# Kernel optimization log

Hardware: AMD Instinct MI355X
Metric: run time of the kernel (lower is better)

The kernel has to match this reference:

```python
import jax, jax.numpy as jnp
import numpy as np

B, L, H, KV, D, HID = 2, 2048, 16, 4, 128, 2048
EPS = 1e-6
ROPE_BASE = 10000.0


def _rotate_half(x):
    x1, x2 = jnp.split(x, 2, axis=-1)
    return jnp.concatenate((-x2, x1), axis=-1)


def _rms_norm(x, w):
    xf = x.astype(jnp.float32)
    var = jnp.mean(xf * xf, axis=-1, keepdims=True)
    return w * (xf * jax.lax.rsqrt(var + EPS)).astype(x.dtype)


def setup_inputs() -> dict:
    key = jax.random.key(0)
    ks = jax.random.split(key, 6)
    hidden_states = jax.random.normal(ks[0], (B, L, HID), dtype=jnp.float32)
    # rotary embeddings (standard rope table)
    inv_freq = 1.0 / (ROPE_BASE ** (jnp.arange(0, D, 2, dtype=jnp.float32) / D))
    pos = jnp.arange(L, dtype=jnp.float32)
    freqs = pos[:, None] * inv_freq[None, :]          # [L, D/2]
    emb = jnp.concatenate((freqs, freqs), axis=-1)    # [L, D]
    cos = jnp.broadcast_to(jnp.cos(emb)[None], (B, L, D))
    sin = jnp.broadcast_to(jnp.sin(emb)[None], (B, L, D))
    s = 0.02
    Wq = jax.random.normal(ks[1], (HID, H * D), dtype=jnp.float32) * s
    Wk = jax.random.normal(ks[2], (HID, KV * D), dtype=jnp.float32) * s
    Wv = jax.random.normal(ks[3], (HID, KV * D), dtype=jnp.float32) * s
    Wo = jax.random.normal(ks[4], (H * D, HID), dtype=jnp.float32) * s
    q_norm_w = jnp.ones((D,), dtype=jnp.float32)
    k_norm_w = jnp.ones((D,), dtype=jnp.float32)
    return {"hidden_states": hidden_states, "cos": cos, "sin": sin,
            "Wq": Wq, "Wk": Wk, "Wv": Wv, "Wo": Wo,
            "q_norm_w": q_norm_w, "k_norm_w": k_norm_w}


def reference(hidden_states, cos, sin, Wq, Wk, Wv, Wo, q_norm_w, k_norm_w):
    scale = D ** -0.5
    n_rep = H // KV
    q = (hidden_states @ Wq).reshape(B, L, H, D)
    k = (hidden_states @ Wk).reshape(B, L, KV, D)
    v = (hidden_states @ Wv).reshape(B, L, KV, D)
    q = _rms_norm(q, q_norm_w).transpose(0, 2, 1, 3)   # [B,H,L,D]
    k = _rms_norm(k, k_norm_w).transpose(0, 2, 1, 3)   # [B,KV,L,D]
    v = v.transpose(0, 2, 1, 3)                         # [B,KV,L,D]
    c = cos[:, None]                                    # [B,1,L,D]
    s = sin[:, None]
    q = q * c + _rotate_half(q) * s
    k = k * c + _rotate_half(k) * s
    # GQA without materializing repeated K/V: group query heads per kv head.
    qg = q.reshape(B, KV, n_rep, L, D)
    scores = jnp.einsum('bgrld,bgmd->bgrlm', qg, k) * scale
    attn = jax.nn.softmax(scores, axis=-1)
    out = jnp.einsum('bgrlm,bgmd->bgrld', attn, v)      # [B,KV,n_rep,L,D]
    out = out.reshape(B, H, L, D).transpose(0, 2, 1, 3).reshape(B, L, H * D)
    return out @ Wo
```

## Files before the change

kernel.cpp:

```cpp
#include <hip/hip_runtime.h>

typedef unsigned short u16;
typedef unsigned int u32;
typedef short bf16x8 __attribute__((ext_vector_type(8)));
typedef float f32x4 __attribute__((ext_vector_type(4)));

#define B_ 2
#define L_ 2048
#define H_ 16
#define KV_ 4
#define D_ 128
#define HID_ 2048

#define QSCALE (0.08838834764831845f * 1.4426950408889634f)

__device__ __forceinline__ u16 f2bf(float f) {
  union { float f; u32 u; } v; v.f = f;
  u32 u = v.u;
  return (u16)((u + 0x7FFFu + ((u >> 16) & 1u)) >> 16);
}
__device__ __forceinline__ float bf2f(u16 h) {
  union { u32 u; float f; } v; v.u = ((u32)h) << 16;
  return v.f;
}
__device__ __forceinline__ u32 pkbf(float a, float b) {
  union { float f; u32 u; } x, y; x.f = a; y.f = b;
  return ((x.u + 0x8000u) >> 16) | ((y.u + 0x8000u) & 0xffff0000u);
}
__device__ __forceinline__ void gl_lds16(const void* g, void* l) {
  __builtin_amdgcn_global_load_lds((__attribute__((address_space(1))) void*)(g),
                                   (__attribute__((address_space(3))) void*)(l),
                                   16, 0, 0);
}

template <int N> __device__ __forceinline__ void vmwait() {
  asm volatile("s_waitcnt vmcnt(%0)" ::"n"(N) : "memory");
}
#define BARRIER()                                                         \
  do {                                                                    \
    asm volatile("" ::: "memory");                                        \
    __builtin_amdgcn_s_barrier();                                         \
    asm volatile("" ::: "memory");                                        \
    __builtin_amdgcn_sched_barrier(0);                                    \
  } while (0)

__global__ void k_prep(const float* __restrict__ hidden, u16* __restrict__ Xb,
                       const float* __restrict__ Wq, const float* __restrict__ Wk,
                       const float* __restrict__ Wv, const float* __restrict__ Wo,
                       u16* __restrict__ Wtqkv, u16* __restrict__ Wto) {
  __shared__ float t[32][33];
  int id = blockIdx.x;
  if (id < 8192) {
    int i = id * 256 + threadIdx.x;
    float4 v = ((const float4*)hidden)[i];
    u32 a = (u32)f2bf(v.x) | ((u32)f2bf(v.y) << 16);
    u32 b = (u32)f2bf(v.z) | ((u32)f2bf(v.w) << 16);
    ((uint2*)Xb)[i] = make_uint2(a, b);
    return;
  }
  id -= 8192;
  const float* src; u16* dst; int C; int ct, rt;
  if (id < 4096)      { src = Wq; dst = Wtqkv;               C = 2048; ct = id & 63; rt = id >> 6; }
  else if (id < 5120) { id -= 4096; src = Wk; dst = Wtqkv + 2048 * 2048; C = 512; ct = id & 15; rt = id >> 4; }
  else if (id < 6144) { id -= 5120; src = Wv; dst = Wtqkv + 2560 * 2048; C = 512; ct = id & 15; rt = id >> 4; }
  else                { id -= 6144; src = Wo; dst = Wto;     C = 2048; ct = id & 63; rt = id >> 6; }
  const int R = 2048;
  int c0 = ct * 32, r0 = rt * 32;
  int tx = threadIdx.x & 31, ty = threadIdx.x >> 5;
  for (int i = ty; i < 32; i += 8)
    t[i][tx] = src[(size_t)(r0 + i) * C + c0 + tx];
  __syncthreads();
  int sc = threadIdx.x >> 3;
  int tg = threadIdx.x & 7;
  u32 lo = (u32)f2bf(t[tg * 4 + 0][sc]) | ((u32)f2bf(t[tg * 4 + 1][sc]) << 16);
  u32 hi = (u32)f2bf(t[tg * 4 + 2][sc]) | ((u32)f2bf(t[tg * 4 + 3][sc]) << 16);
  *(uint2*)(dst + (size_t)(c0 + sc) * R + r0 + tg * 4) = make_uint2(lo, hi);
}

__global__ __launch_bounds__(512, 2) void k_gemm_qkv(
    const u16* __restrict__ A, const u16* __restrict__ Bt,
    const float* __restrict__ cosp, const float* __restrict__ sinp,
    const float* __restrict__ qw, const float* __restrict__ kw,
    u16* __restrict__ Qb, u16* __restrict__ Kb, u16* __restrict__ Vtb) {
  extern __shared__ char smem[];
  const int tid = threadIdx.x;
  const int wave = tid >> 6, lane = tid & 63;
  const int wm = wave >> 2, wn = wave & 3;
  const int quad = lane >> 4, fm = lane & 15;
  const int f7 = fm & 7;

  const int bid = blockIdx.x;
  const int swz = (bid & 7) * 24 + (bid >> 3);
  const int by = swz / 12, bx = swz % 12;
  const int m0 = by * 256, n0 = bx * 256;

  const u16* Ag = A + (size_t)m0 * 2048;
  const u16* Bg = Bt + (size_t)n0 * 2048;
  const int schunk = (lane & 7) ^ ((lane >> 3) & 7);

  f32x4 acc[8][4];
#pragma unroll
  for (int i = 0; i < 8; ++i)
#pragma unroll
    for (int j = 0; j < 4; ++j)
#pragma unroll
      for (int r = 0; r < 4; ++r) acc[i][j][r] = 0.0f;

  bf16x8 af[4][2], bf[4][2];
  const int ArowB = (wm * 128 + fm) * 128;
  const int BrowB = (wn * 64 + fm) * 128;
  const int kc[2] = {(quad ^ f7) * 16, ((quad ^ 4) ^ f7) * 16};

#define STAGE_A(qa_, kk_, bb_)                                               \
  _Pragma("unroll") for (int q = 0; q < 2; ++q) {                            \
    int ldsoff = (bb_)*32768 + q * 16384 + (qa_)*8192 + wave * 1024 + lane * 16; \
    int grow = q * 128 + (qa_)*64 + wave * 8 + (lane >> 3);                  \
    gl_lds16(Ag + (size_t)grow * 2048 + (kk_)*64 + schunk * 8, smem + ldsoff); \
  }
#define STAGE_B(qb_, kk_, bb_)                                               \
  _Pragma("unroll") for (int q = 0; q < 2; ++q) {                            \
    int gg = q * 2 + (wave >> 2);                                            \
    int ldsoff = 65536 + (bb_)*32768 + gg * 8192 + (qb_)*4096 +              \
                 (wave & 3) * 1024 + lane * 16;                              \
    int grow = gg * 64 + (qb_)*32 + (wave & 3) * 8 + (lane >> 3);            \
    gl_lds16(Bg + (size_t)grow * 2048 + (kk_)*64 + schunk * 8, smem + ldsoff); \
  }
#define LDA4(bb_, roff_)                                                     \
  _Pragma("unroll") for (int i = 0; i < 4; ++i)                              \
    _Pragma("unroll") for (int ks = 0; ks < 2; ++ks)                         \
      af[i][ks] = *(const bf16x8*)(smem + (bb_)*32768 + ArowB + (roff_) +    \
                                   i * 2048 + kc[ks]);
#define LDB2(bb_, j0_)                                                       \
  _Pragma("unroll") for (int j = 0; j < 2; ++j)                              \
    _Pragma("unroll") for (int ks = 0; ks < 2; ++ks)                         \
      bf[(j0_) + j][ks] = *(const bf16x8*)(smem + 65536 + (bb_)*32768 +      \
                                           BrowB + ((j0_) + j) * 2048 + kc[ks]);
#define MFMA_Q(I0_, J0_)                                                     \
  __builtin_amdgcn_s_setprio(1);                                             \
  _Pragma("unroll") for (int i = 0; i < 4; ++i)                              \
    _Pragma("unroll") for (int j = 0; j < 2; ++j)                            \
      _Pragma("unroll") for (int ks = 0; ks < 2; ++ks)                       \
        acc[(I0_) + i][(J0_) + j] = __builtin_amdgcn_mfma_f32_16x16x32_bf16( \
            af[i][ks], bf[(J0_) + j][ks], acc[(I0_) + i][(J0_) + j], 0, 0, 0); \
  __builtin_amdgcn_s_setprio(0);
#define TILE(kt_, bb_, ST_, W0_, W1_, W2_)                                   \
  {                                                                          \
    vmwait<W0_>(); BARRIER();                                                \
    LDA4(bb_, 0); LDB2(bb_, 0);                                              \
    if (ST_) { STAGE_A(0, (kt_) + 1, (bb_) ^ 1); }                           \
    MFMA_Q(0, 0);                                                            \
    vmwait<W1_>(); BARRIER();                                                \
    LDB2(bb_, 2);                                                            \
    if (ST_) { STAGE_B(0, (kt_) + 1, (bb_) ^ 1); }                           \
    MFMA_Q(0, 2);                                                            \
    vmwait<W2_>(); BARRIER();                                                \
    LDA4(bb_, 8192);                                                         \
    if (ST_) { STAGE_B(1, (kt_) + 1, (bb_) ^ 1); }                           \
    MFMA_Q(4, 0);                                                            \
    if (ST_) { STAGE_A(1, (kt_) + 1, (bb_) ^ 1); }                           \
    MFMA_Q(4, 2);                                                            \
  }

  STAGE_A(0, 0, 0);
  STAGE_B(0, 0, 0);
  STAGE_B(1, 0, 0);
  STAGE_A(1, 0, 0);

#pragma unroll 1
  for (int t2 = 0; t2 < 30; t2 += 2) {
    TILE(t2, 0, 1, 4, 4, 4);
    TILE(t2 + 1, 1, 1, 4, 4, 4);
  }
  TILE(30, 0, 1, 4, 4, 4);
  TILE(31, 1, 0, 4, 2, 0);

#undef TILE
#undef MFMA_Q
#undef LDB2
#undef LDA4
#undef STAGE_B
#undef STAGE_A

  u16* Cs = (u16*)smem;
  const int head2 = bx * 2;
  const int bL = by >> 3;
  const int l0 = m0 & 2047;
  __syncthreads();
#pragma unroll 1
  for (int qq = 0; qq < 4; ++qq) {
    const int qm = qq >> 1, qn = qq & 1;
    __syncthreads();
    if (wm == qm && (wn >> 1) == qn) {
#pragma unroll
      for (int i = 0; i < 8; ++i)
#pragma unroll
        for (int j = 0; j < 4; ++j)
#pragma unroll
          for (int r = 0; r < 4; ++r)
            Cs[(i * 16 + quad * 4 + r) * 136 + (wn & 1) * 64 + j * 16 + fm] =
                f2bf(acc[i][j][r]);
    }
    __syncthreads();
    const int hq = head2 + qn;
    const int tok0 = m0 + qm * 128;
    const int l0q = l0 + qm * 128;
    if (hq < 20) {
      const int isq = hq < 16;
      const float* wv = isq ? qw : kw;
      const int half = lane >> 5, sl = lane & 31;
      u16* outp = isq ? (Qb + (size_t)(bL * H_ + hq) * L_ * D_)
                      : (Kb + (size_t)(bL * KV_ + hq - 16) * L_ * D_);
      const float4 wvv = *(const float4*)(wv + sl * 4);
      for (int it = 0; it < 8; ++it) {
        int r = wave * 16 + it * 2 + half;
        const u16* crow = Cs + r * 136 + sl * 4;
        u32 c01 = *(const u32*)crow;
        u32 c23 = *(const u32*)(crow + 2);
        float x0 = bf2f((u16)(c01 & 0xffff)), x1 = bf2f((u16)(c01 >> 16));
        float x2 = bf2f((u16)(c23 & 0xffff)), x3 = bf2f((u16)(c23 >> 16));
        float ssq = (x0 * x0 + x1 * x1) + (x2 * x2 + x3 * x3);
        ssq += __shfl_xor(ssq, 1);
        ssq += __shfl_xor(ssq, 2);
        ssq += __shfl_xor(ssq, 4);
        ssq += __shfl_xor(ssq, 8);
        ssq += __shfl_xor(ssq, 16);
        float rr = rsqrtf(ssq * (1.0f / 128.0f) + 1e-6f);
        float nn0 = x0 * rr * wvv.x, nn1 = x1 * rr * wvv.y;
        float nn2 = x2 * rr * wvv.z, nn3 = x3 * rr * wvv.w;
        float p0 = __shfl_xor(nn0, 16), p1 = __shfl_xor(nn1, 16);
        float p2 = __shfl_xor(nn2, 16), p3 = __shfl_xor(nn3, 16);
        float sgn = (sl < 16) ? -1.0f : 1.0f;
        int tok = tok0 + r;
        const float4 cv = *(const float4*)(cosp + (size_t)tok * 128 + sl * 4);
        const float4 sv = *(const float4*)(sinp + (size_t)tok * 128 + sl * 4);
        float o0 = nn0 * cv.x + sgn * p0 * sv.x;
        float o1 = nn1 * cv.y + sgn * p1 * sv.y;
        float o2 = nn2 * cv.z + sgn * p2 * sv.z;
        float o3 = nn3 * cv.w + sgn * p3 * sv.w;
        if (isq) { o0 *= QSCALE; o1 *= QSCALE; o2 *= QSCALE; o3 *= QSCALE; }
        u32 lo = (u32)f2bf(o0) | ((u32)f2bf(o1) << 16);
        u32 hi = (u32)f2bf(o2) | ((u32)f2bf(o3) << 16);
        *(uint2*)(outp + (size_t)(l0q + r) * D_ + sl * 4) = make_uint2(lo, hi);
      }
    } else {
      int g = hq - 20;
      int d = tid >> 2, a2 = (tid >> 1) & 1, lh = tid & 1;
      u16* dst = Vtb + ((size_t)(bL * KV_ + g) * D_ + d) * L_ + l0q + lh * 64;
      for (int bc = 0; bc < 8; ++bc) {
        int b2 = bc & 1, c = bc >> 1;
        int ls = lh * 64 + a2 * 32 + 16 * b2 + 4 * c;
        u32 lo = (u32)Cs[ls * 136 + d] | ((u32)Cs[(ls + 1) * 136 + d] << 16);
        u32 hi = (u32)Cs[(ls + 2) * 136 + d] | ((u32)Cs[(ls + 3) * 136 + d] << 16);
        *(uint2*)(dst + a2 * 32 + 8 * c + 4 * b2) = make_uint2(lo, hi);
      }
    }
  }
}

template <int OUT_BF16>
__global__ __launch_bounds__(256, 3) void k_gemm_bt(
    const u16* __restrict__ A, const u16* __restrict__ Bt, void* __restrict__ Cv,
    int M, int N, int K) {
  __shared__ u16 smem2[16384];
  u16* As = smem2;
  u16* Bs = smem2 + 8192;
  const int tid = threadIdx.x;
  const int wave = tid >> 6, lane = tid & 63;
  const int wr = wave >> 1, wc = wave & 1;
  const int quad = lane >> 4, fm = lane & 15;
  const int m0 = blockIdx.y * 128, n0 = blockIdx.x * 128;
  f32x4 acc[4][4];
  for (int i = 0; i < 4; ++i)
    for (int j = 0; j < 4; ++j)
      for (int r = 0; r < 4; ++r) acc[i][j][r] = 0.0f;

  const int lrow = lane >> 3;
  const int lcol = (lane & 7) * 8;
  const int fk = quad * 8;

  for (int kt = 0; kt < K; kt += 64) {
    for (int p = 0; p < 4; ++p) {
      int roff = wave * 32 + p * 8 + lrow;
      gl_lds16(A + (size_t)(m0 + roff) * K + kt + lcol,
               As + wave * 2048 + p * 512 + lane * 8);
      gl_lds16(Bt + (size_t)(n0 + roff) * K + kt + lcol,
               Bs + wave * 2048 + p * 512 + lane * 8);
    }
    __syncthreads();
    for (int s = 0; s < 2; ++s) {
      bf16x8 af[4], bfr[4];
      for (int i = 0; i < 4; ++i)
        af[i] = *(const bf16x8*)(As + (wr * 64 + i * 16 + fm) * 64 + s * 32 + fk);
      for (int j = 0; j < 4; ++j)
        bfr[j] = *(const bf16x8*)(Bs + (wc * 64 + j * 16 + fm) * 64 + s * 32 + fk);
      for (int i = 0; i < 4; ++i)
        for (int j = 0; j < 4; ++j)
          acc[i][j] = __builtin_amdgcn_mfma_f32_16x16x32_bf16(af[i], bfr[j],
                                                              acc[i][j], 0, 0, 0);
    }
    __syncthreads();
  }

  if (OUT_BF16) {
    u16* Cs = smem2;
    for (int hh = 0; hh < 2; ++hh) {
      if (hh) __syncthreads();
      if (wr == hh)
        for (int i = 0; i < 4; ++i)
          for (int j = 0; j < 4; ++j)
            for (int r = 0; r < 4; ++r)
              Cs[(i * 16 + quad * 4 + r) * 136 + wc * 64 + j * 16 + fm] =
                  f2bf(acc[i][j][r]);
      __syncthreads();
      for (int it = 0; it < 4; ++it) {
        int row = it * 16 + (tid >> 4);
        int col = (tid & 15) * 8;
        uint4 v = *(const uint4*)(Cs + row * 136 + col);
        *(uint4*)((u16*)Cv + (size_t)(m0 + hh * 64 + row) * N + n0 + col) = v;
      }
    }
  } else {
    float* Cf = (float*)Cv;
#pragma unroll
    for (int i = 0; i < 4; ++i)
#pragma unroll
      for (int j = 0; j < 4; ++j)
#pragma unroll
        for (int r = 0; r < 4; ++r)
          Cf[(size_t)(m0 + wr * 64 + i * 16 + quad * 4 + r) * N + n0 + wc * 64 +
             j * 16 + fm] = acc[i][j][r];
  }
}

__global__ __launch_bounds__(256, 2) void k_attn(const u16* __restrict__ Qb,
                                                 const u16* __restrict__ Kb,
                                                 const u16* __restrict__ Vtb,
                                                 u16* __restrict__ AO) {
  __shared__ u16 smem3[32768];
  const int tid = threadIdx.x, wave = tid >> 6, lane = tid & 63;
  const int quad = lane >> 4, fm = lane & 15;
  const int f7 = fm & 7;
  const int bid = blockIdx.x;
  const int xcd = bid & 7, w = bid >> 3;
  const int b = xcd >> 2, g = xcd & 3;
  const int h = g * 4 + (w & 3);
  const int qt = w >> 2;
  const int bh = b * 16 + h;
  const u16* Kg = Kb + ((size_t)(b * KV_ + g)) * L_ * D_;
  const u16* Vg = Vtb + ((size_t)(b * KV_ + g)) * D_ * L_;

  const u16* Qg = Qb + ((size_t)bh * L_ + qt * 128 + wave * 32 + fm) * D_;
  bf16x8 qf1[4], qf2[4];
  for (int ks = 0; ks < 4; ++ks) {
    qf1[ks] = *(const bf16x8*)(Qg + ks * 32 + quad * 8);
    qf2[ks] = *(const bf16x8*)(Qg + 16 * D_ + ks * 32 + quad * 8);
  }

  f32x4 o1[8], o2[8];
  for (int f = 0; f < 8; ++f)
    for (int r = 0; r < 4; ++r) { o1[f][r] = 0.0f; o2[f][r] = 0.0f; }
  float lr1 = 0.0f, lr2 = 0.0f;
  const f32x4 fz = {0.0f, 0.0f, 0.0f, 0.0f};

  const int eK = wave * 2048 + (lane << 3);
  const int cK = lane & 15;
  const int cV = lane & 7;

#define STAGE(kt_, buf_)                                                      \
  {                                                                           \
    u16* Kd = smem3 + (buf_)*16384;                                           \
    u16* Vd = smem3 + (buf_)*16384 + 8192;                                    \
    for (int p = 0; p < 4; ++p) {                                             \
      int e = eK + p * 512;                                                   \
      int rowK = e >> 7;                                                      \
      int gK = (cK & 8) | ((cK & 7) ^ (rowK & 7));                            \
      gl_lds16(Kg + (size_t)((kt_)*64 + rowK) * 128 + gK * 8, Kd + e);        \
      int rowV = e >> 6;                                                      \
      int gV = cV ^ (rowV & 7);                                               \
      gl_lds16(Vg + (size_t)rowV * L_ + (kt_)*64 + gV * 8, Vd + e);           \
    }                                                                         \
  }

  STAGE(0, 0);
  for (int kt = 0; kt < 32; ++kt) {
    __syncthreads();
    if (kt + 1 < 32) STAGE(kt + 1, (kt + 1) & 1);
    const u16* Ks = smem3 + (kt & 1) * 16384;
    const u16* Vs = Ks + 8192;

    f32x4 s1[4], s2[4];
    __builtin_amdgcn_s_setprio(1);
    {
      int cp = (quad & 8) | (quad ^ f7);
      for (int n = 0; n < 4; ++n) {
        bf16x8 kf = *(const bf16x8*)(Ks + (n * 16 + fm) * 128 + cp * 8);
        s1[n] = __builtin_amdgcn_mfma_f32_16x16x32_bf16(kf, qf1[0], fz, 0, 0, 0);
        s2[n] = __builtin_amdgcn_mfma_f32_16x16x32_bf16(kf, qf2[0], fz, 0, 0, 0);
      }
    }
    for (int ks = 1; ks < 4; ++ks) {
      int c = 4 * ks + quad;
      int cp = (c & 8) | ((c & 7) ^ f7);
      for (int n = 0; n < 4; ++n) {
        bf16x8 kf = *(const bf16x8*)(Ks + (n * 16 + fm) * 128 + cp * 8);
        s1[n] = __builtin_amdgcn_mfma_f32_16x16x32_bf16(kf, qf1[ks], s1[n], 0, 0, 0);
        s2[n] = __builtin_amdgcn_mfma_f32_16x16x32_bf16(kf, qf2[ks], s2[n], 0, 0, 0);
      }
    }
    __builtin_amdgcn_s_setprio(0);

    u32 pk1[4][2], pk2[4][2];
    float rs1 = 0.0f, rs2 = 0.0f;
    for (int n = 0; n < 4; ++n) {
      float a0 = __builtin_amdgcn_exp2f(s1[n][0]);
      float a1 = __builtin_amdgcn_exp2f(s1[n][1]);
      float a2 = __builtin_amdgcn_exp2f(s1[n][2]);
      float a3 = __builtin_amdgcn_exp2f(s1[n][3]);
      rs1 += (a0 + a1) + (a2 + a3);
      pk1[n][0] = pkbf(a0, a1);
      pk1[n][1] = pkbf(a2, a3);
      float b0 = __builtin_amdgcn_exp2f(s2[n][0]);
      float b1 = __builtin_amdgcn_exp2f(s2[n][1]);
      float b2 = __builtin_amdgcn_exp2f(s2[n][2]);
      float b3 = __builtin_amdgcn_exp2f(s2[n][3]);
      rs2 += (b0 + b1) + (b2 + b3);
      pk2[n][0] = pkbf(b0, b1);
      pk2[n][1] = pkbf(b2, b3);
    }
    lr1 += rs1;
    lr2 += rs2;

    __builtin_amdgcn_s_setprio(1);
    for (int ks2 = 0; ks2 < 2; ++ks2) {
      union { u32 u[4]; bf16x8 v; } pa1, pa2;
      pa1.u[0] = pk1[2 * ks2][0];
      pa1.u[1] = pk1[2 * ks2][1];
      pa1.u[2] = pk1[2 * ks2 + 1][0];
      pa1.u[3] = pk1[2 * ks2 + 1][1];
      pa2.u[0] = pk2[2 * ks2][0];
      pa2.u[1] = pk2[2 * ks2][1];
      pa2.u[2] = pk2[2 * ks2 + 1][0];
      pa2.u[3] = pk2[2 * ks2 + 1][1];
      int chunk = (4 * ks2 + quad) ^ f7;
      for (int f = 0; f < 8; ++f) {
        bf16x8 vv = *(const bf16x8*)(Vs + (f * 16 + fm) * 64 + chunk * 8);
        o1[f] = __builtin_amdgcn_mfma_f32_16x16x32_bf16(pa1.v, vv, o1[f], 0, 0, 0);
        o2[f] = __builtin_amdgcn_mfma_f32_16x16x32_bf16(pa2.v, vv, o2[f], 0, 0, 0);
      }
    }
    __builtin_amdgcn_s_setprio(0);
  }
#undef STAGE

  const size_t tok0 = (size_t)b * L_ + qt * 128;
  for (int grp = 0; grp < 2; ++grp) {
    f32x4* o = grp ? o2 : o1;
    float lr = grp ? lr2 : lr1;
    lr += __shfl_xor(lr, 16);
    lr += __shfl_xor(lr, 32);
    float li = 1.0f / lr;
    float l0 = __shfl(li, (lane & 48) | (quad * 4 + 0));
    float l1 = __shfl(li, (lane & 48) | (quad * 4 + 1));
    float l2 = __shfl(li, (lane & 48) | (quad * 4 + 2));
    float l3 = __shfl(li, (lane & 48) | (quad * 4 + 3));
    __syncthreads();
    for (int f = 0; f < 8; ++f) {
      int e = (wave * 16 + quad * 4) * 136 + f * 16 + fm;
      smem3[e] = f2bf(o[f][0] * l0);
      smem3[e + 136] = f2bf(o[f][1] * l1);
      smem3[e + 272] = f2bf(o[f][2] * l2);
      smem3[e + 408] = f2bf(o[f][3] * l3);
    }
    __syncthreads();
    for (int it = 0; it < 8; ++it) {
      int crow = (tid >> 6) * 16 + it * 2 + (lane >> 5);
      int q = (crow >> 4) * 32 + grp * 16 + (crow & 15);
      int cc = (lane & 31) * 4;
      uint2 v = *(const uint2*)(smem3 + crow * 136 + cc);
      *(uint2*)(AO + (tok0 + q) * (H_ * D_) + h * D_ + cc) = v;
    }
  }
}

extern "C" void kernel_launch(void* const* d_in, const int* in_sizes, int n_in,
                              void* d_out, int out_size, void* d_ws,
                              size_t ws_size, hipStream_t stream) {
  const float* hidden = (const float*)d_in[0];
  const float* cosp = (const float*)d_in[1];
  const float* sinp = (const float*)d_in[2];
  const float* Wq = (const float*)d_in[3];
  const float* Wk = (const float*)d_in[4];
  const float* Wv = (const float*)d_in[5];
  const float* Wo = (const float*)d_in[6];
  const float* qw = (const float*)d_in[7];
  const float* kw = (const float*)d_in[8];
  float* out = (float*)d_out;

  char* w = (char*)d_ws;
  u16* Xb = (u16*)(w);
  u16* Wtqkv = (u16*)(w + (16u << 20));
  u16* Wto = (u16*)(w + (28u << 20));
  u16* Qb = (u16*)(w + (36u << 20));
  u16* Kb = (u16*)(w + (52u << 20));
  u16* Vtb = (u16*)(w + (56u << 20));
  u16* AO = Xb;

  k_prep<<<18432, 256, 0, stream>>>(hidden, Xb, Wq, Wk, Wv, Wo, Wtqkv, Wto);
  k_gemm_qkv<<<dim3(192), dim3(512), 131072, stream>>>(Xb, Wtqkv, cosp, sinp,
                                                       qw, kw, Qb, Kb, Vtb);
  k_attn<<<dim3(512), 256, 0, stream>>>(Qb, Kb, Vtb, AO);
  k_gemm_bt<0><<<dim3(16, 32), 256, 0, stream>>>(AO, Wto, out, 4096, 2048, 2048);
}
```

Baseline: 306.3 us.

## Move Wo transpose-convert into QKV GEMM launch as extra blocks

The Wo fp32-to-bf16 transpose moves out of the prep kernel and runs as 512 extra blocks appended to the QKV GEMM grid. Those blocks can fill CUs the 192 GEMM blocks leave idle, so the conversion overlaps the GEMM instead of running serially before it. The transpose tile loads in k_prep also switch from scalar loads to float4 loads. The catch is that the extra blocks reserve the GEMM's 128KB dynamic LDS each, which can limit how many fit alongside GEMM blocks, and if they are scheduled ahead of GEMM blocks they may delay them.

Result: faster. 295.5 us (-3.5%).

```diff
diff --git a/kernel.cpp b/kernel.cpp
--- a/kernel.cpp
+++ b/kernel.cpp
@@ -46,8 +46,7 @@
 
 __global__ void k_prep(const float* __restrict__ hidden, u16* __restrict__ Xb,
                        const float* __restrict__ Wq, const float* __restrict__ Wk,
-                       const float* __restrict__ Wv, const float* __restrict__ Wo,
-                       u16* __restrict__ Wtqkv, u16* __restrict__ Wto) {
+                       const float* __restrict__ Wv, u16* __restrict__ Wtqkv) {
   __shared__ float t[32][33];
   int id = blockIdx.x;
   if (id < 8192) {
@@ -62,13 +61,13 @@
   const float* src; u16* dst; int C; int ct, rt;
   if (id < 4096)      { src = Wq; dst = Wtqkv;               C = 2048; ct = id & 63; rt = id >> 6; }
   else if (id < 5120) { id -= 4096; src = Wk; dst = Wtqkv + 2048 * 2048; C = 512; ct = id & 15; rt = id >> 4; }
-  else if (id < 6144) { id -= 5120; src = Wv; dst = Wtqkv + 2560 * 2048; C = 512; ct = id & 15; rt = id >> 4; }
-  else                { id -= 6144; src = Wo; dst = Wto;     C = 2048; ct = id & 63; rt = id >> 6; }
+  else                { id -= 5120; src = Wv; dst = Wtqkv + 2560 * 2048; C = 512; ct = id & 15; rt = id >> 4; }
   const int R = 2048;
   int c0 = ct * 32, r0 = rt * 32;
-  int tx = threadIdx.x & 31, ty = threadIdx.x >> 5;
-  for (int i = ty; i < 32; i += 8)
-    t[i][tx] = src[(size_t)(r0 + i) * C + c0 + tx];
+  int row = threadIdx.x >> 3, c4 = (threadIdx.x & 7) * 4;
+  float4 v = *(const float4*)(src + (size_t)(r0 + row) * C + c0 + c4);
+  t[row][c4 + 0] = v.x; t[row][c4 + 1] = v.y;
+  t[row][c4 + 2] = v.z; t[row][c4 + 3] = v.w;
   __syncthreads();
   int sc = threadIdx.x >> 3;
   int tg = threadIdx.x & 7;
@@ -81,15 +80,42 @@
     const u16* __restrict__ A, const u16* __restrict__ Bt,
     const float* __restrict__ cosp, const float* __restrict__ sinp,
     const float* __restrict__ qw, const float* __restrict__ kw,
-    u16* __restrict__ Qb, u16* __restrict__ Kb, u16* __restrict__ Vtb) {
+    u16* __restrict__ Qb, u16* __restrict__ Kb, u16* __restrict__ Vtb,
+    const float* __restrict__ Wo, u16* __restrict__ Wto) {
   extern __shared__ char smem[];
   const int tid = threadIdx.x;
+  const int bid = blockIdx.x;
+
+  if (bid >= 192) {
+    float (*tt)[32][33] = (float(*)[32][33])smem;
+    const int hf = tid >> 8;
+    const int t2 = tid & 255;
+    const int row = t2 >> 3, c4 = (t2 & 7) * 4;
+    const int sc = t2 >> 3, tg = t2 & 7;
+#pragma unroll 1
+    for (int it = 0; it < 4; ++it) {
+      int tile = (bid - 192) * 8 + it * 2 + hf;
+      int ct = tile & 63, rt = tile >> 6;
+      int c0 = ct * 32, r0 = rt * 32;
+      float4 v = *(const float4*)(Wo + (size_t)(r0 + row) * 2048 + c0 + c4);
+      __syncthreads();
+      tt[hf][row][c4 + 0] = v.x; tt[hf][row][c4 + 1] = v.y;
+      tt[hf][row][c4 + 2] = v.z; tt[hf][row][c4 + 3] = v.w;
+      __syncthreads();
+      u32 lo = (u32)f2bf(tt[hf][tg * 4 + 0][sc]) |
+               ((u32)f2bf(tt[hf][tg * 4 + 1][sc]) << 16);
+      u32 hi = (u32)f2bf(tt[hf][tg * 4 + 2][sc]) |
+               ((u32)f2bf(tt[hf][tg * 4 + 3][sc]) << 16);
+      *(uint2*)(Wto + (size_t)(c0 + sc) * 2048 + r0 + tg * 4) = make_uint2(lo, hi);
+    }
+    return;
+  }
+
   const int wave = tid >> 6, lane = tid & 63;
   const int wm = wave >> 2, wn = wave & 3;
   const int quad = lane >> 4, fm = lane & 15;
   const int f7 = fm & 7;
 
-  const int bid = blockIdx.x;
   const int swz = (bid & 7) * 24 + (bid >> 3);
   const int by = swz / 12, bx = swz % 12;
   const int m0 = by * 256, n0 = bx * 256;
@@ -505,9 +531,10 @@
   u16* Vtb = (u16*)(w + (56u << 20));
   u16* AO = Xb;
 
-  k_prep<<<18432, 256, 0, stream>>>(hidden, Xb, Wq, Wk, Wv, Wo, Wtqkv, Wto);
-  k_gemm_qkv<<<dim3(192), dim3(512), 131072, stream>>>(Xb, Wtqkv, cosp, sinp,
-                                                       qw, kw, Qb, Kb, Vtb);
+  k_prep<<<14336, 256, 0, stream>>>(hidden, Xb, Wq, Wk, Wv, Wtqkv);
+  k_gemm_qkv<<<dim3(704), dim3(512), 131072, stream>>>(Xb, Wtqkv, cosp, sinp,
+                                                       qw, kw, Qb, Kb, Vtb,
+                                                       Wo, Wto);
   k_attn<<<dim3(512), 256, 0, stream>>>(Qb, Kb, Vtb, AO);
   k_gemm_bt<0><<<dim3(16, 32), 256, 0, stream>>>(AO, Wto, out, 4096, 2048, 2048);
 }
```
